# Kernel optimization log

Hardware: AMD Instinct MI355X
Metric: run time of the kernel (lower is better)

Reference implementation:

```python
import jax, jax.numpy as jnp
import numpy as np

EPS = 1e-12
N_HEADS = 16


def _ln(x, g, b, eps=EPS):
    m = jnp.mean(x, axis=-1, keepdims=True)
    v = jnp.var(x, axis=-1, keepdims=True)
    return (x - m) * jax.lax.rsqrt(v + eps) * g + b


def setup_inputs() -> dict:
    key = jax.random.key(0)
    ks = jax.random.split(key, 8)
    B, S, D, I = 2, 2048, 1024, 4096
    s = 0.02
    f32 = jnp.float32
    return {
        "x": jax.random.normal(ks[0], (B, S, D), f32),
        "input_mask": jnp.zeros((B, 1, 1, S), f32),  # additive mask, 0 = no masking
        "norm_w": jnp.ones((D,), f32),
        "norm_b": jnp.zeros((D,), f32),
        "attn_qkvw": jax.random.normal(ks[1], (D, 3 * D), f32) * s,
        "attn_qkvb": jnp.zeros((3 * D,), f32),
        "attn_ow": jax.random.normal(ks[2], (D, D), f32) * s,
        "attn_ob": jnp.zeros((D,), f32),
        "attn_nw": jnp.ones((D,), f32),
        "attn_nb": jnp.zeros((D,), f32),
        "inter_w": jax.random.normal(ks[3], (D, I), f32) * s,
        "inter_b": jnp.zeros((I,), f32),
        "inter_w1": jax.random.normal(ks[4], (D, I), f32) * s,
        "output_w": jax.random.normal(ks[5], (I, D), f32) * s,
        "output_b": jnp.zeros((D,), f32),
    }


def reference(x, input_mask, norm_w, norm_b, attn_qkvw, attn_qkvb, attn_ow,
              attn_ob, attn_nw, attn_nb, inter_w, inter_b, inter_w1,
              output_w, output_b):
    B, S, D = x.shape
    hd = D // N_HEADS

    # --- fused qkv_gemm: pre-layernorm + QKV GEMM + bias ---
    ln1 = _ln(x, norm_w, norm_b)
    qkv = ln1 @ attn_qkvw + attn_qkvb            # [B,S,3D]
    q, k, v = jnp.split(qkv, 3, axis=-1)

    def to_heads(t):  # [B,S,D] -> [B,H,S,hd]
        return t.reshape(B, S, N_HEADS, hd).transpose(0, 2, 1, 3)

    q, k, v = to_heads(q), to_heads(k), to_heads(v)

    # --- softmax-context attention (scale_attention=True -> 1/sqrt(head_dim)) ---
    scores = jnp.einsum('bhqd,bhkd->bhqk', q, k) / jnp.sqrt(jnp.float32(hd))
    scores = scores + input_mask                 # additive mask [B,1,1,S]
    probs = jax.nn.softmax(scores, axis=-1)
    ctx = jnp.einsum('bhqk,bhkd->bhqd', probs, v)
    ctx = ctx.transpose(0, 2, 1, 3).reshape(B, S, D)

    attn_out = ctx @ attn_ow                     # vector_matmul (no bias)

    # --- fused mlp_gemm: bias+residual add, layernorm, GEMM+bias+gelu ---
    residual_add = attn_out + attn_ob + x
    ln2 = _ln(residual_add, attn_nw, attn_nb)
    intermediate = jax.nn.gelu(ln2 @ inter_w + inter_b, approximate=False)
    # gated path: vector_matmul(mlp input, inter_w1) * intermediate (per source)
    intermediate = (attn_out @ inter_w1) * intermediate

    # --- output projection + bias_residual ---
    out = intermediate @ output_w + output_b + residual_add
    return out
```

## Files before the change

### kernel.cpp

```cpp
#include <hip/hip_runtime.h>
#include <hip/hip_bf16.h>

#define BATCH 2
#define SEQ   2048
#define DIM   1024
#define IDIM  4096
#define NH    16
#define HD    64
#define TOK   (BATCH * SEQ)

typedef __hip_bfloat16 bf16;

typedef short bf16x8_t __attribute__((ext_vector_type(8)));
typedef float f32x4_t  __attribute__((ext_vector_type(4)));

__device__ __forceinline__ float ldv(const float* p, size_t i) { return p[i]; }
__device__ __forceinline__ float ldv(const bf16*  p, size_t i) { return __bfloat162float(p[i]); }
__device__ __forceinline__ void  stv(float* p, size_t i, float v) { p[i] = v; }
__device__ __forceinline__ void  stv(bf16*  p, size_t i, float v) { p[i] = __float2bfloat16(v); }

__device__ __forceinline__ f32x4_t mfma16(bf16x8_t a, bf16x8_t b, f32x4_t c) {
    return __builtin_amdgcn_mfma_f32_16x16x32_bf16(a, b, c, 0, 0, 0);
}

__device__ __forceinline__ void gload16(const bf16* g, bf16* l) {
    __builtin_amdgcn_global_load_lds(
        (const __attribute__((address_space(1))) void*)g,
        (__attribute__((address_space(3))) void*)l, 16, 0, 0);
}

__device__ __forceinline__ void xcd_map(int &bx, int &by) {
    const int gn  = gridDim.x;
    const int lin = blockIdx.y * gn + blockIdx.x;
    const int cx  = gn >> 3;
    const int xcd = lin & 7;
    const int slot = lin >> 3;
    bx = xcd * cx + slot % cx;
    by = slot / cx;
}

__global__ __launch_bounds__(256) void ln_kernel(const float* __restrict__ in,
                                                 const float* __restrict__ w,
                                                 const float* __restrict__ b,
                                                 bf16* __restrict__ out) {
    const int row = blockIdx.x;
    const int tid = threadIdx.x;
    const float* xr = in + (size_t)row * DIM;

    float v[4], sum = 0.f, sq = 0.f;
#pragma unroll
    for (int i = 0; i < 4; i++) {
        float t = xr[tid + i * 256];
        v[i] = t; sum += t; sq += t * t;
    }
#pragma unroll
    for (int off = 32; off >= 1; off >>= 1) {
        sum += __shfl_xor(sum, off);
        sq  += __shfl_xor(sq,  off);
    }
    __shared__ float s1[4], s2[4];
    int wid = tid >> 6;
    if ((tid & 63) == 0) { s1[wid] = sum; s2[wid] = sq; }
    __syncthreads();
    sum = s1[0] + s1[1] + s1[2] + s1[3];
    sq  = s2[0] + s2[1] + s2[2] + s2[3];

    const float mean = sum * (1.f / DIM);
    const float var  = fmaxf(sq * (1.f / DIM) - mean * mean, 0.f);
    const float rstd = rsqrtf(var + 1e-12f);

    bf16* orow = out + (size_t)row * DIM;
#pragma unroll
    for (int i = 0; i < 4; i++) {
        int idx = tid + i * 256;
        orow[idx] = __float2bfloat16((v[i] - mean) * rstd * w[idx] + b[idx]);
    }
}

__global__ __launch_bounds__(256) void wconv_kernel(const float* __restrict__ W,
                                                    bf16* __restrict__ Wt,
                                                    int K, int N) {
    __shared__ float tile[32][33];
    const int tid = threadIdx.x;
    const int n0 = blockIdx.x * 32;
    const int k0 = blockIdx.y * 32;
    const int c = tid & 31;
    const int r = tid >> 5;
#pragma unroll
    for (int i = 0; i < 4; i++)
        tile[r + i * 8][c] = W[(size_t)(k0 + r + i * 8) * N + n0 + c];
    __syncthreads();
#pragma unroll
    for (int i = 0; i < 4; i++)
        Wt[(size_t)(n0 + r + i * 8) * K + k0 + c] = __float2bfloat16(tile[c][r + i * 8]);
}

#define GBK 32

template<typename TX, int MODE, int TM, int TN>
__global__ __launch_bounds__(256) void mgemm_kernel(const bf16* __restrict__ A,
                                                    const bf16* __restrict__ Bt,
                                                    const float* __restrict__ bias,
                                                    const TX* __restrict__ aux,
                                                    TX* __restrict__ C,
                                                    const float* __restrict__ bias2,
                                                    const float* __restrict__ xin,
                                                    float* __restrict__ C2,
                                                    int M, int N, int K) {
    constexpr int TILE_M = TM * 32;
    constexpr int TILE_N = TN * 32;
    __shared__ alignas(16) bf16 As[2][TILE_M][GBK];
    __shared__ alignas(16) bf16 Bs[2][TILE_N][GBK];

    const int tid  = threadIdx.x;
    const int w    = tid >> 6;
    const int lane = tid & 63;
    const int cl   = lane & 15;
    const int qd   = lane >> 4;
    const int wm   = w >> 1;
    const int wn   = w & 1;

    int bx, by;
    xcd_map(bx, by);

    const int row0 = by * TILE_M;
    const int col0 = bx * TILE_N;

    const int lrow = lane >> 2;
    const int lkg  = lane & 3;
    const int sslot = lkg ^ ((lrow >> 1) & 3);
    const int rds   = (cl >> 1) & 3;

    const bf16* gA = A  + (size_t)(row0 + lrow) * K + sslot * 8;
    const bf16* gB = Bt + (size_t)(col0 + lrow) * K + sslot * 8;

    f32x4_t acc[TM][TN];
#pragma unroll
    for (int m = 0; m < TM; m++)
#pragma unroll
        for (int n = 0; n < TN; n++) acc[m][n] = {0.f, 0.f, 0.f, 0.f};

    auto stage = [&](int b, int k0) {
#pragma unroll
        for (int i = 0; i < TM / 2; i++) {
            const int r16 = (w * (TM / 2) + i) * 16;
            gload16(gA + (size_t)r16 * K + k0, &As[b][r16][0]);
        }
#pragma unroll
        for (int j = 0; j < TN / 2; j++) {
            const int r16 = (w * (TN / 2) + j) * 16;
            gload16(gB + (size_t)r16 * K + k0, &Bs[b][r16][0]);
        }
    };

    stage(0, 0);
    __syncthreads();

    const int NT = K / GBK;
    for (int t = 0; t < NT; t++) {
        const int b = t & 1;
        if (t + 1 < NT) stage(b ^ 1, (t + 1) * GBK);

        bf16x8_t af[TM], bfr[TN];
#pragma unroll
        for (int m = 0; m < TM; m++)
            af[m] = *(const bf16x8_t*)&As[b][wm * (TM * 16) + m * 16 + cl][(qd ^ rds) * 8];
#pragma unroll
        for (int n = 0; n < TN; n++)
            bfr[n] = *(const bf16x8_t*)&Bs[b][wn * (TN * 16) + n * 16 + cl][(qd ^ rds) * 8];
#pragma unroll
        for (int m = 0; m < TM; m++)
#pragma unroll
            for (int n = 0; n < TN; n++)
                acc[m][n] = mfma16(af[m], bfr[n], acc[m][n]);

        __syncthreads();
    }

#pragma unroll
    for (int m = 0; m < TM; m++) {
#pragma unroll
        for (int n = 0; n < TN; n++) {
            const int gc = col0 + wn * (TN * 16) + n * 16 + cl;
            const float bv = (MODE != 4 && bias) ? bias[gc] : 0.f;
#pragma unroll
            for (int r = 0; r < 4; r++) {
                const int gr = row0 + wm * (TM * 16) + m * 16 + qd * 4 + r;
                float c = acc[m][n][r] + bv;
                if (MODE == 3) {
                    c += ldv(aux, (size_t)gr * N + gc);
                }
                stv(C, (size_t)gr * N + gc, c);
                if (MODE == 4) {
                    C2[(size_t)gr * N + gc] = c + bias2[gc] + xin[(size_t)gr * N + gc];
                }
            }
        }
    }
}

template<int TM, int TN>
__global__ __launch_bounds__(256) void dualgemm_kernel(const bf16* __restrict__ A0,
                                                       const bf16* __restrict__ B0t,
                                                       const bf16* __restrict__ A1,
                                                       const bf16* __restrict__ B1t,
                                                       const float* __restrict__ bias,
                                                       bf16* __restrict__ C,
                                                       int M, int N, int K) {
    constexpr int TILE_M = TM * 32;
    constexpr int TILE_N = TN * 32;
    __shared__ alignas(16) bf16 As0[2][TILE_M][GBK];
    __shared__ alignas(16) bf16 Bs0[2][TILE_N][GBK];
    __shared__ alignas(16) bf16 As1[2][TILE_M][GBK];
    __shared__ alignas(16) bf16 Bs1[2][TILE_N][GBK];

    const int tid  = threadIdx.x;
    const int w    = tid >> 6;
    const int lane = tid & 63;
    const int cl   = lane & 15;
    const int qd   = lane >> 4;
    const int wm   = w >> 1;
    const int wn   = w & 1;

    int bx, by;
    xcd_map(bx, by);

    const int row0 = by * TILE_M;
    const int col0 = bx * TILE_N;

    const int lrow = lane >> 2;
    const int lkg  = lane & 3;
    const int sslot = lkg ^ ((lrow >> 1) & 3);
    const int rds   = (cl >> 1) & 3;

    const bf16* gA0 = A0  + (size_t)(row0 + lrow) * K + sslot * 8;
    const bf16* gB0 = B0t + (size_t)(col0 + lrow) * K + sslot * 8;
    const bf16* gA1 = A1  + (size_t)(row0 + lrow) * K + sslot * 8;
    const bf16* gB1 = B1t + (size_t)(col0 + lrow) * K + sslot * 8;

    f32x4_t acc0[TM][TN], acc1[TM][TN];
#pragma unroll
    for (int m = 0; m < TM; m++)
#pragma unroll
        for (int n = 0; n < TN; n++) {
            acc0[m][n] = {0.f, 0.f, 0.f, 0.f};
            acc1[m][n] = {0.f, 0.f, 0.f, 0.f};
        }

    auto stage = [&](int b, int k0) {
#pragma unroll
        for (int i = 0; i < TM / 2; i++) {
            const int r16 = (w * (TM / 2) + i) * 16;
            gload16(gA0 + (size_t)r16 * K + k0, &As0[b][r16][0]);
            gload16(gA1 + (size_t)r16 * K + k0, &As1[b][r16][0]);
        }
#pragma unroll
        for (int j = 0; j < TN / 2; j++) {
            const int r16 = (w * (TN / 2) + j) * 16;
            gload16(gB0 + (size_t)r16 * K + k0, &Bs0[b][r16][0]);
            gload16(gB1 + (size_t)r16 * K + k0, &Bs1[b][r16][0]);
        }
    };

    stage(0, 0);
    __syncthreads();

    const int NT = K / GBK;
    for (int t = 0; t < NT; t++) {
        const int b = t & 1;
        if (t + 1 < NT) stage(b ^ 1, (t + 1) * GBK);

        bf16x8_t af0[TM], af1[TM];
#pragma unroll
        for (int m = 0; m < TM; m++) {
            const int rr = wm * (TM * 16) + m * 16 + cl;
            af0[m] = *(const bf16x8_t*)&As0[b][rr][(qd ^ rds) * 8];
            af1[m] = *(const bf16x8_t*)&As1[b][rr][(qd ^ rds) * 8];
        }
#pragma unroll
        for (int n = 0; n < TN; n++) {
            const int rr = wn * (TN * 16) + n * 16 + cl;
            bf16x8_t b0 = *(const bf16x8_t*)&Bs0[b][rr][(qd ^ rds) * 8];
            bf16x8_t b1 = *(const bf16x8_t*)&Bs1[b][rr][(qd ^ rds) * 8];
#pragma unroll
            for (int m = 0; m < TM; m++) {
                acc0[m][n] = mfma16(af0[m], b0, acc0[m][n]);
                acc1[m][n] = mfma16(af1[m], b1, acc1[m][n]);
            }
        }

        __syncthreads();
    }

#pragma unroll
    for (int m = 0; m < TM; m++) {
#pragma unroll
        for (int n = 0; n < TN; n++) {
            const int gc = col0 + wn * (TN * 16) + n * 16 + cl;
            const float bv = bias[gc];
#pragma unroll
            for (int r = 0; r < 4; r++) {
                const int gr = row0 + wm * (TM * 16) + m * 16 + qd * 4 + r;
                float g = acc0[m][n][r] + bv;
                g = 0.5f * g * (1.f + erff(g * 0.70710678118654752f));
                C[(size_t)gr * N + gc] = __float2bfloat16(g * acc1[m][n][r]);
            }
        }
    }
}

__global__ __launch_bounds__(256) void vtrans_kernel(const bf16* __restrict__ qkv,
                                                     bf16* __restrict__ vt) {
    __shared__ bf16 t[64][72];
    const int tid = threadIdx.x;
    const int s0  = blockIdx.x * 64;
    const int bh  = blockIdx.y;
    const int bb  = bh >> 4;
    const int h   = bh & 15;
    const bf16* src = qkv + (size_t)bb * SEQ * (3 * DIM) + 2 * DIM + h * HD;
    const int r  = tid >> 3;
    const int cc = tid & 7;
#pragma unroll
    for (int i = 0; i < 2; i++)
        *(bf16x8_t*)&t[r + i * 32][cc * 8] =
            *(const bf16x8_t*)(src + (size_t)(s0 + r + i * 32) * (3 * DIM) + cc * 8);
    __syncthreads();
    bf16* dst = vt + (size_t)bh * HD * SEQ + s0;
#pragma unroll
    for (int i = 0; i < 2; i++) {
        const int d = r + i * 32;
        bf16x8_t v;
#pragma unroll
        for (int j = 0; j < 8; j++)
            ((short*)&v)[j] = *(const short*)&t[cc * 8 + j][d];
        *(bf16x8_t*)(dst + (size_t)d * SEQ + cc * 8) = v;
    }
}

#define KCH 64
#define NCH (SEQ / KCH)

__device__ __forceinline__ unsigned pk2(float lo, float hi) {
    unsigned a = (unsigned)__bfloat16_as_ushort(__float2bfloat16(lo));
    unsigned b = (unsigned)__bfloat16_as_ushort(__float2bfloat16(hi));
    return a | (b << 16);
}

union PAU { bf16x8_t v; unsigned u[4]; };

__global__ __launch_bounds__(256, 2) void attn_mfma_kernel(const bf16* __restrict__ qkv,
                                                           const bf16* __restrict__ vt,
                                                           const float* __restrict__ mask,
                                                           bf16* __restrict__ ctx) {
    __shared__ alignas(16) bf16 Kl[2][KCH][64];
    __shared__ alignas(16) bf16 Vl[2][KCH][64];

    const int tid  = threadIdx.x;
    const int w    = tid >> 6;
    const int lane = tid & 63;
    const int cl   = lane & 15;
    const int qd   = lane >> 4;
    const int c7   = cl & 7;

    const int qtile = blockIdx.x;
    const int bh    = blockIdx.y;
    const int bb    = bh >> 4;
    const int h     = bh & 15;

    const bf16*  base = qkv + (size_t)bb * SEQ * (3 * DIM) + h * HD;
    const bf16*  gK   = base + DIM;
    const bf16*  gV   = vt + (size_t)bh * HD * SEQ;
    const float* mrow = mask + (size_t)bb * SEQ;

    bf16x8_t aq[2][2];
#pragma unroll
    for (int qt = 0; qt < 2; qt++) {
        const bf16* qrow = base + (size_t)(qtile * 128 + w * 32 + qt * 16 + cl) * (3 * DIM);
        aq[qt][0] = *(const bf16x8_t*)(qrow + qd * 8);
        aq[qt][1] = *(const bf16x8_t*)(qrow + 32 + qd * 8);
    }

    const bf16x8_t onesv = {0x3F80, 0x3F80, 0x3F80, 0x3F80,
                            0x3F80, 0x3F80, 0x3F80, 0x3F80};

    const int sr  = lane >> 3;
    const int scw = (lane & 7) ^ sr;

#pragma unroll
    for (int i = 0; i < 2; i++) {
        const int row = i * 32 + w * 8 + sr;
        gload16(gK + (size_t)row * (3 * DIM) + scw * 8, &Kl[0][i * 32 + w * 8][0]);
        gload16(gV + (size_t)row * SEQ + scw * 8, &Vl[0][i * 32 + w * 8][0]);
    }
    f32x4_t mkx[4];
#pragma unroll
    for (int ks = 0; ks < 4; ks++)
        mkx[ks] = *(const f32x4_t*)&mrow[ks * 16 + qd * 4];

    f32x4_t O[2][4];
#pragma unroll
    for (int qt = 0; qt < 2; qt++)
#pragma unroll
        for (int ns = 0; ns < 4; ns++) O[qt][ns] = {0.f, 0.f, 0.f, 0.f};
    f32x4_t li[2] = {{0.f,0.f,0.f,0.f},{0.f,0.f,0.f,0.f}};

    for (int c = 0; c < NCH; c++) {
        __syncthreads();
        const bf16 (*Kb)[64] = Kl[c & 1];
        const bf16 (*Vb)[64] = Vl[c & 1];

        f32x4_t mk[4];
#pragma unroll
        for (int ks = 0; ks < 4; ks++) mk[ks] = mkx[ks];

        if (c + 1 < NCH) {
            bf16 (*Kn)[64] = Kl[(c + 1) & 1];
            bf16 (*Vn)[64] = Vl[(c + 1) & 1];
            const int k0n = (c + 1) * KCH;
#pragma unroll
            for (int i = 0; i < 2; i++) {
                const int row = i * 32 + w * 8 + sr;
                gload16(gK + (size_t)(k0n + row) * (3 * DIM) + scw * 8, &Kn[i * 32 + w * 8][0]);
                gload16(gV + (size_t)row * SEQ + k0n + scw * 8, &Vn[i * 32 + w * 8][0]);
            }
#pragma unroll
            for (int ks = 0; ks < 4; ks++)
                mkx[ks] = *(const f32x4_t*)&mrow[k0n + ks * 16 + qd * 4];
        }

        bf16x8_t kf[4][2];
#pragma unroll
        for (int ks = 0; ks < 4; ks++) {
            kf[ks][0] = *(const bf16x8_t*)&Kb[ks * 16 + cl][(qd ^ c7) << 3];
            kf[ks][1] = *(const bf16x8_t*)&Kb[ks * 16 + cl][((4 + qd) ^ c7) << 3];
        }

        PAU pa[2][2];
#pragma unroll
        for (int qt = 0; qt < 2; qt++) {
            unsigned Dv[4][2];
#pragma unroll
            for (int ks = 0; ks < 4; ks++) {
                f32x4_t s = {0.f, 0.f, 0.f, 0.f};
                s = mfma16(kf[ks][0], aq[qt][0], s);
                s = mfma16(kf[ks][1], aq[qt][1], s);
                const float e0 = __expf(s[0] * 0.125f + mk[ks][0]);
                const float e1 = __expf(s[1] * 0.125f + mk[ks][1]);
                const float e2 = __expf(s[2] * 0.125f + mk[ks][2]);
                const float e3 = __expf(s[3] * 0.125f + mk[ks][3]);
                Dv[ks][0] = pk2(e0, e1);
                Dv[ks][1] = pk2(e2, e3);
            }
#pragma unroll
            for (int rp = 0; rp < 2; rp++) {
                auto z0 = __builtin_amdgcn_permlane32_swap(Dv[0][rp], Dv[1][rp], false, false);
                auto w0 = __builtin_amdgcn_permlane16_swap(z0[0], z0[1], false, false);
                pa[qt][0].u[rp]     = w0[0];
                pa[qt][0].u[rp + 2] = w0[1];
                auto z1 = __builtin_amdgcn_permlane32_swap(Dv[2][rp], Dv[3][rp], false, false);
                auto w1 = __builtin_amdgcn_permlane16_swap(z1[0], z1[1], false, false);
                pa[qt][1].u[rp]     = w1[0];
                pa[qt][1].u[rp + 2] = w1[1];
            }
            f32x4_t ls = {0.f, 0.f, 0.f, 0.f};
            ls = mfma16(pa[qt][0].v, onesv, ls);
            ls = mfma16(pa[qt][1].v, onesv, ls);
            li[qt] += ls;
        }

#pragma unroll
        for (int ns = 0; ns < 4; ns++) {
            bf16x8_t v0 = *(const bf16x8_t*)&Vb[ns * 16 + cl][(qd ^ c7) << 3];
            bf16x8_t v1 = *(const bf16x8_t*)&Vb[ns * 16 + cl][((4 + qd) ^ c7) << 3];
#pragma unroll
            for (int qt = 0; qt < 2; qt++) {
                O[qt][ns] = mfma16(pa[qt][0].v, v0, O[qt][ns]);
                O[qt][ns] = mfma16(pa[qt][1].v, v1, O[qt][ns]);
            }
        }
    }

#pragma unroll
    for (int qt = 0; qt < 2; qt++) {
#pragma unroll
        for (int r = 0; r < 4; r++) {
            const int row = qtile * 128 + w * 32 + qt * 16 + qd * 4 + r;
            bf16* orow = ctx + (size_t)(bb * SEQ + row) * DIM + h * HD;
            const float inv = 1.f / li[qt][r];
#pragma unroll
            for (int ns = 0; ns < 4; ns++)
                orow[ns * 16 + cl] = __float2bfloat16(O[qt][ns][r] * inv);
        }
    }
}

extern "C" void kernel_launch(void* const* d_in, const int* in_sizes, int n_in,
                              void* d_out, int out_size, void* d_ws, size_t ws_size,
                              hipStream_t stream) {
    const float* x        = (const float*)d_in[0];
    const float* mask     = (const float*)d_in[1];
    const float* norm_w   = (const float*)d_in[2];
    const float* norm_b   = (const float*)d_in[3];
    const float* qkvw     = (const float*)d_in[4];
    const float* qkvb     = (const float*)d_in[5];
    const float* attn_ow  = (const float*)d_in[6];
    const float* attn_ob  = (const float*)d_in[7];
    const float* attn_nw  = (const float*)d_in[8];
    const float* attn_nb  = (const float*)d_in[9];
    const float* inter_w  = (const float*)d_in[10];
    const float* inter_b  = (const float*)d_in[11];
    const float* inter_w1 = (const float*)d_in[12];
    const float* output_w = (const float*)d_in[13];
    const float* output_b = (const float*)d_in[14];

    float* out = (float*)d_out;
    bf16*  ws  = (bf16*)d_ws;

    const size_t M1 = 1024 * 1024;
    bf16* ln_s      = ws;
    bf16* qkv       = ws + 4 * M1;
    bf16* inter     = ws + 4 * M1;
    bf16* qkvw_t    = ws + 16 * M1;
    bf16* attn_owt  = ws + 19 * M1;
    bf16* vt        = ws + 20 * M1;
    bf16* attn_out  = ws + 20 * M1;
    bf16* inter_wt  = ws + 24 * M1;
    bf16* inter_w1t = ws + 28 * M1;
    bf16* output_wt = ws + 32 * M1;
    float* resid    = out;

    dim3 blk(256);

    wconv_kernel<<<dim3(3072 / 32, 1024 / 32), blk, 0, stream>>>(qkvw,     qkvw_t,    1024, 3072);
    wconv_kernel<<<dim3(1024 / 32, 1024 / 32), blk, 0, stream>>>(attn_ow,  attn_owt,  1024, 1024);
    wconv_kernel<<<dim3(4096 / 32, 1024 / 32), blk, 0, stream>>>(inter_w,  inter_wt,  1024, 4096);
    wconv_kernel<<<dim3(4096 / 32, 1024 / 32), blk, 0, stream>>>(inter_w1, inter_w1t, 1024, 4096);
    wconv_kernel<<<dim3(1024 / 32, 4096 / 32), blk, 0, stream>>>(output_w, output_wt, 4096, 1024);

    ln_kernel<<<TOK, blk, 0, stream>>>(x, norm_w, norm_b, ln_s);

    mgemm_kernel<bf16, 0, 4, 4><<<dim3(3072 / 128, TOK / 128), blk, 0, stream>>>(
        ln_s, qkvw_t, qkvb, (const bf16*)nullptr, qkv,
        nullptr, nullptr, nullptr, TOK, 3 * DIM, DIM);

    vtrans_kernel<<<dim3(SEQ / 64, BATCH * NH), blk, 0, stream>>>(qkv, vt);

    attn_mfma_kernel<<<dim3(SEQ / 128, BATCH * NH), blk, 0, stream>>>(qkv, vt, mask, ln_s);

    mgemm_kernel<bf16, 4, 4, 2><<<dim3(DIM / 64, TOK / 128), blk, 0, stream>>>(
        ln_s, attn_owt, (const float*)nullptr, (const bf16*)nullptr, attn_out,
        attn_ob, x, resid, TOK, DIM, DIM);

    ln_kernel<<<TOK, blk, 0, stream>>>(resid, attn_nw, attn_nb, ln_s);

    dualgemm_kernel<4, 4><<<dim3(IDIM / 128, TOK / 128), blk, 0, stream>>>(
        ln_s, inter_wt, attn_out, inter_w1t, inter_b, inter, TOK, IDIM, DIM);

    mgemm_kernel<float, 3, 4, 2><<<dim3(DIM / 64, TOK / 128), blk, 0, stream>>>(
        inter, output_wt, output_b, resid, out,
        nullptr, nullptr, nullptr, TOK, DIM, IDIM);
}
```

Baseline: 499.1 us.

## Deepen GEMM prefetch to two tiles ahead with explicit waitcnt barriers

After: 495.9 us. About the same (-0.6%).

```diff
diff --git a/kernel.cpp b/kernel.cpp
--- a/kernel.cpp
+++ b/kernel.cpp
@@ -109,6 +109,7 @@
                                                     int M, int N, int K) {
     constexpr int TILE_M = TM * 32;
     constexpr int TILE_N = TN * 32;
+    constexpr int LOADS  = TM / 2 + TN / 2;
     __shared__ alignas(16) bf16 As[2][TILE_M][GBK];
     __shared__ alignas(16) bf16 Bs[2][TILE_N][GBK];
 
@@ -154,27 +155,42 @@
     };
 
     stage(0, 0);
-    __syncthreads();
+    stage(1, GBK);
+    asm volatile("s_waitcnt vmcnt(%0)" :: "i"(LOADS) : "memory");
+    __builtin_amdgcn_s_barrier();
 
     const int NT = K / GBK;
     for (int t = 0; t < NT; t++) {
-        const int b = t & 1;
-        if (t + 1 < NT) stage(b ^ 1, (t + 1) * GBK);
+        const int cur = t & 1;
 
         bf16x8_t af[TM], bfr[TN];
 #pragma unroll
         for (int m = 0; m < TM; m++)
-            af[m] = *(const bf16x8_t*)&As[b][wm * (TM * 16) + m * 16 + cl][(qd ^ rds) * 8];
+            af[m] = *(const bf16x8_t*)&As[cur][wm * (TM * 16) + m * 16 + cl][(qd ^ rds) * 8];
 #pragma unroll
         for (int n = 0; n < TN; n++)
-            bfr[n] = *(const bf16x8_t*)&Bs[b][wn * (TN * 16) + n * 16 + cl][(qd ^ rds) * 8];
+            bfr[n] = *(const bf16x8_t*)&Bs[cur][wn * (TN * 16) + n * 16 + cl][(qd ^ rds) * 8];
+        asm volatile("s_waitcnt lgkmcnt(0)" ::: "memory");
+        __builtin_amdgcn_sched_barrier(0);
+        __builtin_amdgcn_s_barrier();
+
+        if (t + 2 < NT) stage(cur, (t + 2) * GBK);
+
+        __builtin_amdgcn_s_setprio(1);
 #pragma unroll
         for (int m = 0; m < TM; m++)
 #pragma unroll
             for (int n = 0; n < TN; n++)
                 acc[m][n] = mfma16(af[m], bfr[n], acc[m][n]);
-
-        __syncthreads();
+        __builtin_amdgcn_s_setprio(0);
+
+        if (t + 1 < NT) {
+            if (t + 2 < NT)
+                asm volatile("s_waitcnt vmcnt(%0)" :: "i"(LOADS) : "memory");
+            else
+                asm volatile("s_waitcnt vmcnt(0)" ::: "memory");
+            __builtin_amdgcn_s_barrier();
+        }
     }
 
 #pragma unroll
@@ -209,6 +225,7 @@
                                                        int M, int N, int K) {
     constexpr int TILE_M = TM * 32;
     constexpr int TILE_N = TN * 32;
+    constexpr int LOADS  = TM + TN;
     __shared__ alignas(16) bf16 As0[2][TILE_M][GBK];
     __shared__ alignas(16) bf16 Bs0[2][TILE_N][GBK];
     __shared__ alignas(16) bf16 As1[2][TILE_M][GBK];
@@ -263,33 +280,50 @@
     };
 
     stage(0, 0);
-    __syncthreads();
+    stage(1, GBK);
+    asm volatile("s_waitcnt vmcnt(%0)" :: "i"(LOADS) : "memory");
+    __builtin_amdgcn_s_barrier();
 
     const int NT = K / GBK;
     for (int t = 0; t < NT; t++) {
-        const int b = t & 1;
-        if (t + 1 < NT) stage(b ^ 1, (t + 1) * GBK);
-
-        bf16x8_t af0[TM], af1[TM];
+        const int cur = t & 1;
+
+        bf16x8_t af0[TM], af1[TM], bf0[TN], bf1[TN];
 #pragma unroll
         for (int m = 0; m < TM; m++) {
             const int rr = wm * (TM * 16) + m * 16 + cl;
-            af0[m] = *(const bf16x8_t*)&As0[b][rr][(qd ^ rds) * 8];
-            af1[m] = *(const bf16x8_t*)&As1[b][rr][(qd ^ rds) * 8];
+            af0[m] = *(const bf16x8_t*)&As0[cur][rr][(qd ^ rds) * 8];
+            af1[m] = *(const bf16x8_t*)&As1[cur][rr][(qd ^ rds) * 8];
         }
 #pragma unroll
         for (int n = 0; n < TN; n++) {
             const int rr = wn * (TN * 16) + n * 16 + cl;
-            bf16x8_t b0 = *(const bf16x8_t*)&Bs0[b][rr][(qd ^ rds) * 8];
-            bf16x8_t b1 = *(const bf16x8_t*)&Bs1[b][rr][(qd ^ rds) * 8];
+            bf0[n] = *(const bf16x8_t*)&Bs0[cur][rr][(qd ^ rds) * 8];
+            bf1[n] = *(const bf16x8_t*)&Bs1[cur][rr][(qd ^ rds) * 8];
+        }
+        asm volatile("s_waitcnt lgkmcnt(0)" ::: "memory");
+        __builtin_amdgcn_sched_barrier(0);
+        __builtin_amdgcn_s_barrier();
+
+        if (t + 2 < NT) stage(cur, (t + 2) * GBK);
+
+        __builtin_amdgcn_s_setprio(1);
+#pragma unroll
+        for (int n = 0; n < TN; n++)
 #pragma unroll
             for (int m = 0; m < TM; m++) {
-                acc0[m][n] = mfma16(af0[m], b0, acc0[m][n]);
-                acc1[m][n] = mfma16(af1[m], b1, acc1[m][n]);
-            }
-        }
-
-        __syncthreads();
+                acc0[m][n] = mfma16(af0[m], bf0[n], acc0[m][n]);
+                acc1[m][n] = mfma16(af1[m], bf1[n], acc1[m][n]);
+            }
+        __builtin_amdgcn_s_setprio(0);
+
+        if (t + 1 < NT) {
+            if (t + 2 < NT)
+                asm volatile("s_waitcnt vmcnt(%0)" :: "i"(LOADS) : "memory");
+            else
+                asm volatile("s_waitcnt vmcnt(0)" ::: "memory");
+            __builtin_amdgcn_s_barrier();
+        }
     }
 
 #pragma unroll
```
